# Optimization experiments

Hardware: AMD Instinct MI355X
Metric: run time of the kernel (lower is better)

## Reference

```python
import jax, jax.numpy as jnp
import numpy as np

N, E, D, H = 50000, 800000, 64, 64  # nodes, edges, feat dim, hidden dim
EPS = 1e-3  # Keras BatchNormalization default epsilon

def bn(x, g, b, mu, v):
    # inference-mode batch norm with moving statistics
    return (x - mu) * jax.lax.rsqrt(v + EPS) * g + b

def gelu(x):
    return jax.nn.gelu(x, approximate=False)  # tf.nn.gelu default is exact

def setup_inputs() -> dict:
    key = jax.random.key(0)
    ks = jax.random.split(key, 24)
    r = lambda i, shape, s=1.0: (jax.random.normal(ks[i], shape, jnp.float32) * s)
    inp = {
        "node_feats": r(0, (N, D)),
        "edge_feats": r(1, (E, D)),
        "src": jax.random.randint(ks[2], (E,), 0, N, jnp.int32),
        "dst": jax.random.randint(ks[3], (E,), 0, N, jnp.int32),
        # message MLP (BN -> Dense(gelu)) x2, input D
        "m_g1": 1.0 + 0.1 * r(4, (D,)), "m_b1": 0.1 * r(5, (D,)),
        "m_mu1": 0.1 * r(6, (D,)), "m_v1": jnp.ones((D,), jnp.float32),
        "m_W1": r(7, (D, H), 1.0 / np.sqrt(D)), "m_c1": jnp.zeros((H,), jnp.float32),
        "m_g2": 1.0 + 0.1 * r(8, (H,)), "m_b2": 0.1 * r(9, (H,)),
        "m_mu2": 0.1 * r(10, (H,)), "m_v2": jnp.ones((H,), jnp.float32),
        "m_W2": r(11, (H, H), 1.0 / np.sqrt(H)), "m_c2": jnp.zeros((H,), jnp.float32),
        # edge transformer MLP (Dense(gelu)) x2, input D
        "e_W1": r(12, (D, H), 1.0 / np.sqrt(D)), "e_c1": jnp.zeros((H,), jnp.float32),
        "e_W2": r(13, (H, H), 1.0 / np.sqrt(H)), "e_c2": jnp.zeros((H,), jnp.float32),
        # update MLP (BN -> Dense(gelu)) x2, input D+H (concat combination)
        "u_g1": 1.0 + 0.1 * r(14, (D + H,)), "u_b1": 0.1 * r(15, (D + H,)),
        "u_mu1": 0.1 * r(16, (D + H,)), "u_v1": jnp.ones((D + H,), jnp.float32),
        "u_W1": r(17, (D + H, H), 1.0 / np.sqrt(D + H)), "u_c1": jnp.zeros((H,), jnp.float32),
        "u_g2": 1.0 + 0.1 * r(18, (H,)), "u_b2": 0.1 * r(19, (H,)),
        "u_mu2": 0.1 * r(20, (H,)), "u_v2": jnp.ones((H,), jnp.float32),
        "u_W2": r(21, (H, H), 1.0 / np.sqrt(H)), "u_c2": jnp.zeros((H,), jnp.float32),
    }
    return inp

def reference(node_feats, edge_feats,
              m_g1, m_b1, m_mu1, m_v1, m_W1, m_c1,
              m_g2, m_b2, m_mu2, m_v2, m_W2, m_c2,
              e_W1, e_c1, e_W2, e_c2,
              u_g1, u_b1, u_mu1, u_v1, u_W1, u_c1,
              u_g2, u_b2, u_mu2, u_v2, u_W2, u_c2,
              src, dst):
    # gather neighbour representations: [E, D]
    nbr = node_feats[dst]
    # base message MLP: (BN -> Dropout(identity at inference) -> Dense gelu) x2
    h = gelu(bn(nbr, m_g1, m_b1, m_mu1, m_v1) @ m_W1 + m_c1)
    msg = gelu(bn(h, m_g2, m_b2, m_mu2, m_v2) @ m_W2 + m_c2)
    # edge transformer: Dense(gelu) x2, gates the messages elementwise
    er = gelu(edge_feats @ e_W1 + e_c1)
    er = gelu(er @ e_W2 + e_c2)
    msg = msg * er  # [E, H]
    # unsorted_segment_mean over source node indices (empty segments -> 0)
    s = jax.ops.segment_sum(msg, src, num_segments=N)
    cnt = jax.ops.segment_sum(jnp.ones((E, 1), msg.dtype), src, num_segments=N)
    agg = s / jnp.maximum(cnt, 1.0)  # [N, H]
    # combine ('concat') and update MLP
    hcat = jnp.concatenate([node_feats, agg], axis=-1)  # [N, D+H]
    h = gelu(bn(hcat, u_g1, u_b1, u_mu1, u_v1) @ u_W1 + u_c1)
    out = gelu(bn(h, u_g2, u_b2, u_mu2, u_v2) @ u_W2 + u_c2)
    return out  # [N, H]
```

## Files before the change

kernel.cpp:

```cpp
#include <hip/hip_runtime.h>
#include <hip/hip_bf16.h>

#define NN 50000
#define NE 800000

typedef __bf16 bf16_t;
typedef bf16_t bf16x8 __attribute__((ext_vector_type(8)));
typedef float f32x4 __attribute__((ext_vector_type(4)));

__device__ __forceinline__ float gelu_f(float x) {
    float v = x * fmaf(x * x, 0.07135481627f, 1.595769122f);
    float e = __expf(-v);
    return x * __builtin_amdgcn_rcpf(1.0f + e);
}

__device__ void fold_frag(int K, const float* W, const float* g, const float* b,
                          const float* mu, const float* v, const float* c,
                          bf16_t* Wf, float* cb, int tid, float* part) {
    const int n = tid & 63, kc = tid >> 6;
    const int nt = n >> 4, lrow = n & 15, nkc = K >> 5;
    const int kq = K >> 2, k0 = kc * kq, k1 = k0 + kq;
    float acc = 0.f;
    for (int k = k0; k < k1; ++k) {
        float w = W[k * 64 + n];
        float s = 1.0f, o = 0.0f;
        if (g) {
            s = g[k] * __frsqrt_rn(v[k] + 1e-3f);
            o = b[k] - mu[k] * s;
        }
        int idx = ((nt * nkc + (k >> 5)) * 64 + ((k >> 3) & 3) * 16 + lrow) * 8 + (k & 7);
        Wf[idx] = (bf16_t)(w * s);
        acc += o * w;
    }
    part[kc * 64 + n] = acc;
    __syncthreads();
    if (kc == 0) cb[n] = c[n] + part[n] + part[64 + n] + part[128 + n] + part[192 + n];
}

__global__ void fold_kernel(
    const float* mg1, const float* mb1, const float* mmu1, const float* mv1,
    const float* mW1, const float* mc1,
    const float* mg2, const float* mb2, const float* mmu2, const float* mv2,
    const float* mW2, const float* mc2,
    const float* eW1, const float* ec1, const float* eW2, const float* ec2,
    const float* ug1, const float* ub1, const float* umu1, const float* uv1,
    const float* uW1, const float* uc1,
    const float* ug2, const float* ub2, const float* umu2, const float* uv2,
    const float* uW2, const float* uc2,
    bf16_t* wcat, bf16_t* uW1f, bf16_t* uW2f,
    float* cm1, float* cm2, float* ce1, float* ce2, float* cu1, float* cu2)
{
    __shared__ float part[256];
    int t = threadIdx.x;
    switch (blockIdx.x) {
        case 0: fold_frag(64,  mW1, mg1, mb1, mmu1, mv1, mc1, wcat,         cm1, t, part); break;
        case 1: fold_frag(64,  mW2, mg2, mb2, mmu2, mv2, mc2, wcat + 4096,  cm2, t, part); break;
        case 2: fold_frag(64,  eW1, nullptr, nullptr, nullptr, nullptr, ec1, wcat + 8192,  ce1, t, part); break;
        case 3: fold_frag(64,  eW2, nullptr, nullptr, nullptr, nullptr, ec2, wcat + 12288, ce2, t, part); break;
        case 4: fold_frag(128, uW1, ug1, ub1, umu1, uv1, uc1, uW1f, cu1, t, part); break;
        case 5: fold_frag(64,  uW2, ug2, ub2, umu2, uv2, uc2, uW2f, cu2, t, part); break;
    }
}

__global__ void hist_kernel(const int* __restrict__ src, int* __restrict__ cnt) {
    int e = blockIdx.x * 256 + threadIdx.x;
    if (e < NE) atomicAdd(&cnt[src[e]], 1);
}

__global__ void scanA_kernel(const int* __restrict__ cnt, int* __restrict__ part,
                             int* __restrict__ btot) {
    __shared__ int s[256];
    int tid = threadIdx.x;
    int i = blockIdx.x * 256 + tid;
    int v = (i < NN) ? cnt[i] : 0;
    s[tid] = v;
    __syncthreads();
    #pragma unroll
    for (int off = 1; off < 256; off <<= 1) {
        int t = (tid >= off) ? s[tid - off] : 0;
        __syncthreads();
        s[tid] += t;
        __syncthreads();
    }
    if (i < NN) part[i] = s[tid] - v;
    if (tid == 255) btot[blockIdx.x] = s[255];
}

__global__ void scanB_kernel(int* __restrict__ btot, int nblk) {
    __shared__ int s[256];
    int tid = threadIdx.x;
    int v = (tid < nblk) ? btot[tid] : 0;
    s[tid] = v;
    __syncthreads();
    #pragma unroll
    for (int off = 1; off < 256; off <<= 1) {
        int t = (tid >= off) ? s[tid - off] : 0;
        __syncthreads();
        s[tid] += t;
        __syncthreads();
    }
    if (tid < nblk) btot[tid] = s[tid] - v;
}

__global__ void scanC_kernel(const int* __restrict__ part, const int* __restrict__ btot,
                             int* __restrict__ woff) {
    int i = blockIdx.x * 256 + threadIdx.x;
    if (i < NN) woff[i] = part[i] + btot[i >> 8];
}

__global__ void fill_kernel(const int* __restrict__ src, int* __restrict__ woff,
                            int* __restrict__ elist) {
    int e = blockIdx.x * 256 + threadIdx.x;
    if (e < NE) {
        int pos = atomicAdd(&woff[src[e]], 1);
        elist[pos] = e;
    }
}

__device__ __forceinline__ void mk_frag_hilo(const float* row, int quad,
        bf16x8& hi0, bf16x8& lo0, bf16x8& hi1, bf16x8& lo1)
{
    #pragma unroll
    for (int j = 0; j < 8; ++j) {
        float x0 = row[quad * 8 + j];
        float x1 = row[32 + quad * 8 + j];
        bf16_t h0 = (bf16_t)x0, h1 = (bf16_t)x1;
        hi0[j] = h0; lo0[j] = (bf16_t)(x0 - (float)h0);
        hi1[j] = h1; lo1[j] = (bf16_t)(x1 - (float)h1);
    }
}

__device__ __forceinline__ bf16x8 ldb(const bf16_t* wf, int slot, int lane) {
    return *(const bf16x8*)(wf + (slot * 64 + lane) * 8);
}

__device__ __forceinline__ void gemm64_hilo(const bf16_t* wf, int m,
        bf16x8 h0, bf16x8 l0, bf16x8 h1, bf16x8 l1, f32x4 (&acc)[4], int lane)
{
    #pragma unroll
    for (int nt = 0; nt < 4; ++nt) {
        bf16x8 b0 = ldb(wf, m * 8 + nt * 2 + 0, lane);
        bf16x8 b1 = ldb(wf, m * 8 + nt * 2 + 1, lane);
        f32x4 c = {0.f, 0.f, 0.f, 0.f};
        c = __builtin_amdgcn_mfma_f32_16x16x32_bf16(h0, b0, c, 0, 0, 0);
        c = __builtin_amdgcn_mfma_f32_16x16x32_bf16(l0, b0, c, 0, 0, 0);
        c = __builtin_amdgcn_mfma_f32_16x16x32_bf16(h1, b1, c, 0, 0, 0);
        c = __builtin_amdgcn_mfma_f32_16x16x32_bf16(l1, b1, c, 0, 0, 0);
        acc[nt] = c;
    }
}

__device__ __forceinline__ void gemm64(const bf16_t* wf, int m,
        bf16x8 a0, bf16x8 a1, f32x4 (&acc)[4], int lane)
{
    #pragma unroll
    for (int nt = 0; nt < 4; ++nt) {
        bf16x8 b0 = ldb(wf, m * 8 + nt * 2 + 0, lane);
        bf16x8 b1 = ldb(wf, m * 8 + nt * 2 + 1, lane);
        f32x4 c = {0.f, 0.f, 0.f, 0.f};
        c = __builtin_amdgcn_mfma_f32_16x16x32_bf16(a0, b0, c, 0, 0, 0);
        c = __builtin_amdgcn_mfma_f32_16x16x32_bf16(a1, b1, c, 0, 0, 0);
        acc[nt] = c;
    }
}

__device__ __forceinline__ void epi_to_frag(const f32x4 (&acc)[4], const float* bias,
        bf16_t* h, int lrow, int quad)
{
    #pragma unroll
    for (int nt = 0; nt < 4; ++nt) {
        float bb = bias[nt * 16 + lrow];
        #pragma unroll
        for (int r = 0; r < 4; ++r)
            h[((nt * 2 + (lrow >> 3)) * 16 + quad * 4 + r) * 8 + (lrow & 7)] =
                (bf16_t)gelu_f(acc[nt][r] + bb);
    }
}

__global__ __launch_bounds__(256) void edge_kernel(
    const float* __restrict__ node_feats, const float* __restrict__ edge_feats,
    const int* __restrict__ src, const int* __restrict__ dst,
    const bf16_t* __restrict__ wcat,
    const float* __restrict__ cm1, const float* __restrict__ cm2,
    const float* __restrict__ ce1, const float* __restrict__ ce2,
    float* __restrict__ s_acc, bf16_t* __restrict__ buf, int use_csr)
{
    __shared__ bf16_t wf[16384];
    __shared__ bf16_t hf[4][1024];

    const int tid  = threadIdx.x;
    const int wave = tid >> 6;
    const int lane = tid & 63;
    const int quad = lane >> 4;
    const int lrow = lane & 15;

    #pragma unroll
    for (int i = 0; i < 8; ++i) {
        int chunk = tid + i * 256;
        *(bf16x8*)(wf + chunk * 8) = *(const bf16x8*)(wcat + chunk * 8);
    }
    __syncthreads();

    const int ebase = blockIdx.x * 64 + wave * 16;
    bf16_t* h = hf[wave];

    f32x4 acc[4];

    {
        const float* erow = edge_feats + (size_t)(ebase + lrow) * 64;
        bf16x8 h0, l0, h1, l1;
        mk_frag_hilo(erow, quad, h0, l0, h1, l1);
        gemm64_hilo(wf, 2, h0, l0, h1, l1, acc, lane);
        epi_to_frag(acc, ce1, h, lrow, quad);
    }
    float er[4][4];
    {
        bf16x8 a0 = *(const bf16x8*)(h + lane * 8);
        bf16x8 a1 = *(const bf16x8*)(h + (lane + 64) * 8);
        gemm64(wf, 3, a0, a1, acc, lane);
        #pragma unroll
        for (int nt = 0; nt < 4; ++nt) {
            float bb = ce2[nt * 16 + lrow];
            #pragma unroll
            for (int r = 0; r < 4; ++r) er[nt][r] = gelu_f(acc[nt][r] + bb);
        }
    }

    {
        const int dnode = dst[ebase + lrow];
        const float* nrow = node_feats + (size_t)dnode * 64;
        bf16x8 h0, l0, h1, l1;
        mk_frag_hilo(nrow, quad, h0, l0, h1, l1);
        gemm64_hilo(wf, 0, h0, l0, h1, l1, acc, lane);
        epi_to_frag(acc, cm1, h, lrow, quad);
    }
    float msg[4][4];
    {
        bf16x8 a0 = *(const bf16x8*)(h + lane * 8);
        bf16x8 a1 = *(const bf16x8*)(h + (lane + 64) * 8);
        gemm64(wf, 1, a0, a1, acc, lane);
        #pragma unroll
        for (int nt = 0; nt < 4; ++nt) {
            float bb = cm2[nt * 16 + lrow];
            #pragma unroll
            for (int r = 0; r < 4; ++r) msg[nt][r] = gelu_f(acc[nt][r] + bb);
        }
    }

    if (use_csr) {
        #pragma unroll
        for (int r = 0; r < 4; ++r) {
            bf16_t* bp = buf + (size_t)(ebase + quad * 4 + r) * 64;
            #pragma unroll
            for (int nt = 0; nt < 4; ++nt)
                bp[nt * 16 + lrow] = (bf16_t)(msg[nt][r] * er[nt][r]);
        }
    } else {
        #pragma unroll
        for (int r = 0; r < 4; ++r) {
            float* srow = s_acc + (size_t)src[ebase + quad * 4 + r] * 64;
            #pragma unroll
            for (int nt = 0; nt < 4; ++nt)
                unsafeAtomicAdd(srow + nt * 16 + lrow, msg[nt][r] * er[nt][r]);
        }
    }
}

__global__ __launch_bounds__(256) void agg_kernel(
    const bf16_t* __restrict__ buf, const int* __restrict__ elist,
    const int* __restrict__ woff, const int* __restrict__ cnt,
    float* __restrict__ agg)
{
    const int wave = threadIdx.x >> 6;
    const int lane = threadIdx.x & 63;
    const int n = blockIdx.x * 4 + wave;
    const int deg = cnt[n];
    const int end = woff[n];
    const int start = end - deg;

    float s0 = 0.f, s1 = 0.f, s2 = 0.f, s3 = 0.f;
    int j = start;
    for (; j + 4 <= end; j += 4) {
        int e0 = elist[j], e1 = elist[j + 1], e2 = elist[j + 2], e3 = elist[j + 3];
        s0 += (float)buf[(size_t)e0 * 64 + lane];
        s1 += (float)buf[(size_t)e1 * 64 + lane];
        s2 += (float)buf[(size_t)e2 * 64 + lane];
        s3 += (float)buf[(size_t)e3 * 64 + lane];
    }
    for (; j < end; ++j)
        s0 += (float)buf[(size_t)elist[j] * 64 + lane];

    float r = (deg > 0) ? (s0 + s1 + s2 + s3) * __builtin_amdgcn_rcpf((float)deg) : 0.f;
    agg[(size_t)n * 64 + lane] = r;
}

__global__ __launch_bounds__(256) void update_kernel(
    const float* __restrict__ node_feats,
    const float* __restrict__ aggv, const int* __restrict__ cnt,
    const bf16_t* __restrict__ uW1f, const float* __restrict__ cu1,
    const bf16_t* __restrict__ uW2f, const float* __restrict__ cu2,
    float* __restrict__ out)
{
    __shared__ bf16_t w1f[8192];
    __shared__ bf16_t w2f[4096];
    __shared__ bf16_t hf[4][1024];

    const int tid  = threadIdx.x;
    const int wave = tid >> 6;
    const int lane = tid & 63;
    const int quad = lane >> 4;
    const int lrow = lane & 15;

    #pragma unroll
    for (int i = 0; i < 4; ++i) {
        int chunk = tid + i * 256;
        *(bf16x8*)(w1f + chunk * 8) = *(const bf16x8*)(uW1f + chunk * 8);
    }
    #pragma unroll
    for (int i = 0; i < 2; ++i) {
        int chunk = tid + i * 256;
        *(bf16x8*)(w2f + chunk * 8) = *(const bf16x8*)(uW2f + chunk * 8);
    }
    __syncthreads();

    const int nbase = blockIdx.x * 64 + wave * 16;
    int arow = nbase + lrow;
    arow = arow < NN ? arow : NN - 1;

    const float* nf   = node_feats + (size_t)arow * 64;
    const float* srow = aggv + (size_t)arow * 64;
    float inv = cnt ? 1.0f / fmaxf((float)cnt[arow], 1.0f) : 1.0f;

    bf16x8 ah[4], al[4];
    #pragma unroll
    for (int j = 0; j < 8; ++j) {
        float x0 = nf[quad * 8 + j];
        float x1 = nf[32 + quad * 8 + j];
        float x2 = srow[quad * 8 + j] * inv;
        float x3 = srow[32 + quad * 8 + j] * inv;
        bf16_t h0 = (bf16_t)x0, h1 = (bf16_t)x1, h2 = (bf16_t)x2, h3 = (bf16_t)x3;
        ah[0][j] = h0; al[0][j] = (bf16_t)(x0 - (float)h0);
        ah[1][j] = h1; al[1][j] = (bf16_t)(x1 - (float)h1);
        ah[2][j] = h2; al[2][j] = (bf16_t)(x2 - (float)h2);
        ah[3][j] = h3; al[3][j] = (bf16_t)(x3 - (float)h3);
    }

    f32x4 acc[4];
    #pragma unroll
    for (int nt = 0; nt < 4; ++nt) {
        f32x4 c = {0.f, 0.f, 0.f, 0.f};
        #pragma unroll
        for (int kk = 0; kk < 4; ++kk) {
            bf16x8 b = *(const bf16x8*)(w1f + ((nt * 4 + kk) * 64 + lane) * 8);
            c = __builtin_amdgcn_mfma_f32_16x16x32_bf16(ah[kk], b, c, 0, 0, 0);
            c = __builtin_amdgcn_mfma_f32_16x16x32_bf16(al[kk], b, c, 0, 0, 0);
        }
        acc[nt] = c;
    }
    bf16_t* hb = hf[wave];
    epi_to_frag(acc, cu1, hb, lrow, quad);

    bf16x8 ha0 = *(const bf16x8*)(hb + lane * 8);
    bf16x8 ha1 = *(const bf16x8*)(hb + (lane + 64) * 8);
    gemm64(w2f, 0, ha0, ha1, acc, lane);

    #pragma unroll
    for (int nt = 0; nt < 4; ++nt) {
        int col = nt * 16 + lrow;
        float bb = cu2[col];
        #pragma unroll
        for (int r = 0; r < 4; ++r) {
            int row = nbase + quad * 4 + r;
            if (row < NN)
                out[(size_t)row * 64 + col] = gelu_f(acc[nt][r] + bb);
        }
    }
}

extern "C" void kernel_launch(void* const* d_in, const int* in_sizes, int n_in,
                              void* d_out, int out_size, void* d_ws, size_t ws_size,
                              hipStream_t stream) {
    const float* node_feats = (const float*)d_in[0];
    const float* edge_feats = (const float*)d_in[1];
    const int*   src        = (const int*)d_in[2];
    const int*   dst        = (const int*)d_in[3];

    char* ws = (char*)d_ws;
    const bool csr = ws_size >= (size_t)119200000;

    size_t off = 0;
    bf16_t* buf = nullptr; float* agg = nullptr; int* elist = nullptr;
    int* cnt = nullptr; int* woff = nullptr; int* part = nullptr; int* btot = nullptr;
    float* s_acc = nullptr;

    if (csr) {
        buf   = (bf16_t*)(ws + off); off += (size_t)NE * 64 * 2;
        agg   = (float*)(ws + off);  off += (size_t)NN * 64 * 4;
        elist = (int*)(ws + off);    off += (size_t)NE * 4;
        cnt   = (int*)(ws + off);    off += (size_t)NN * 4;
        woff  = (int*)(ws + off);    off += (size_t)NN * 4;
        part  = (int*)(ws + off);    off += (size_t)NN * 4;
        btot  = (int*)(ws + off);    off += 1024;
    } else {
        s_acc = (float*)(ws + off);  off += (size_t)NN * 64 * 4;
        cnt   = (int*)(ws + off);    off += (size_t)NN * 4;
    }
    bf16_t* wcat = (bf16_t*)(ws + off); off += 32768;
    bf16_t* uW1f = (bf16_t*)(ws + off); off += 16384;
    bf16_t* uW2f = (bf16_t*)(ws + off); off += 8192;
    float* cm1 = (float*)(ws + off); off += 256;
    float* cm2 = (float*)(ws + off); off += 256;
    float* ce1 = (float*)(ws + off); off += 256;
    float* ce2 = (float*)(ws + off); off += 256;
    float* cu1 = (float*)(ws + off); off += 256;
    float* cu2 = (float*)(ws + off); off += 256;

    if (csr) {
        hipMemsetAsync(cnt, 0, (size_t)NN * 4, stream);
    } else {
        hipMemsetAsync(s_acc, 0, (size_t)NN * 64 * 4 + (size_t)NN * 4, stream);
    }

    fold_kernel<<<6, 256, 0, stream>>>(
        (const float*)d_in[4],  (const float*)d_in[5],  (const float*)d_in[6],  (const float*)d_in[7],
        (const float*)d_in[8],  (const float*)d_in[9],
        (const float*)d_in[10], (const float*)d_in[11], (const float*)d_in[12], (const float*)d_in[13],
        (const float*)d_in[14], (const float*)d_in[15],
        (const float*)d_in[16], (const float*)d_in[17], (const float*)d_in[18], (const float*)d_in[19],
        (const float*)d_in[20], (const float*)d_in[21], (const float*)d_in[22], (const float*)d_in[23],
        (const float*)d_in[24], (const float*)d_in[25],
        (const float*)d_in[26], (const float*)d_in[27], (const float*)d_in[28], (const float*)d_in[29],
        (const float*)d_in[30], (const float*)d_in[31],
        wcat, uW1f, uW2f, cm1, cm2, ce1, ce2, cu1, cu2);

    hist_kernel<<<(NE + 255) / 256, 256, 0, stream>>>(src, cnt);

    if (csr) {
        const int NBLK = (NN + 255) / 256;
        scanA_kernel<<<NBLK, 256, 0, stream>>>(cnt, part, btot);
        scanB_kernel<<<1, 256, 0, stream>>>(btot, NBLK);
        scanC_kernel<<<NBLK, 256, 0, stream>>>(part, btot, woff);
        fill_kernel<<<(NE + 255) / 256, 256, 0, stream>>>(src, woff, elist);
    }

    edge_kernel<<<NE / 64, 256, 0, stream>>>(
        node_feats, edge_feats, src, dst,
        wcat, cm1, cm2, ce1, ce2, s_acc, buf, csr ? 1 : 0);

    if (csr) {
        agg_kernel<<<NN / 4, 256, 0, stream>>>(buf, elist, woff, cnt, agg);
        update_kernel<<<(NN + 63) / 64, 256, 0, stream>>>(
            node_feats, agg, nullptr, uW1f, cu1, uW2f, cu2, (float*)d_out);
    } else {
        update_kernel<<<(NN + 63) / 64, 256, 0, stream>>>(
            node_feats, s_acc, cnt, uW1f, cu1, uW2f, cu2, (float*)d_out);
    }
}
```

Baseline: 563.5 us.

## Compute message MLP per node and scatter edge outputs into CSR order

The message MLP depends only on the destination node's features, so a new node_msg_kernel computes it once per node (50k rows instead of 800k edges) and stores it as bf16. The edge kernel then gathers that precomputed bf16 message, runs only the edge-transformer MLP, and writes the gated product straight to its CSR slot using a per-edge position from fill_kernel. The aggregation kernel can then read contiguous rows with no edge-list indirection. In exchange the node messages are rounded to bf16 before gating, and pos and msg share workspace with agg.

```diff
diff --git a/kernel.cpp b/kernel.cpp
--- a/kernel.cpp
+++ b/kernel.cpp
@@ -109,12 +109,9 @@
 }
 
 __global__ void fill_kernel(const int* __restrict__ src, int* __restrict__ woff,
-                            int* __restrict__ elist) {
+                            int* __restrict__ pos) {
     int e = blockIdx.x * 256 + threadIdx.x;
-    if (e < NE) {
-        int pos = atomicAdd(&woff[src[e]], 1);
-        elist[pos] = e;
-    }
+    if (e < NE) pos[e] = atomicAdd(&woff[src[e]], 1);
 }
 
 __device__ __forceinline__ void mk_frag_hilo(const float* row, int quad,
@@ -177,15 +174,12 @@
     }
 }
 
-__global__ __launch_bounds__(256) void edge_kernel(
-    const float* __restrict__ node_feats, const float* __restrict__ edge_feats,
-    const int* __restrict__ src, const int* __restrict__ dst,
-    const bf16_t* __restrict__ wcat,
+__global__ __launch_bounds__(256) void node_msg_kernel(
+    const float* __restrict__ node_feats, const bf16_t* __restrict__ wcat,
     const float* __restrict__ cm1, const float* __restrict__ cm2,
-    const float* __restrict__ ce1, const float* __restrict__ ce2,
-    float* __restrict__ s_acc, bf16_t* __restrict__ buf, int use_csr)
-{
-    __shared__ bf16_t wf[16384];
+    bf16_t* __restrict__ msg)
+{
+    __shared__ bf16_t wf[8192];
     __shared__ bf16_t hf[4][1024];
 
     const int tid  = threadIdx.x;
@@ -195,81 +189,121 @@
     const int lrow = lane & 15;
 
     #pragma unroll
-    for (int i = 0; i < 8; ++i) {
+    for (int i = 0; i < 4; ++i) {
         int chunk = tid + i * 256;
         *(bf16x8*)(wf + chunk * 8) = *(const bf16x8*)(wcat + chunk * 8);
     }
     __syncthreads();
 
+    const int nbase = blockIdx.x * 64 + wave * 16;
+    int arow = nbase + lrow;
+    arow = arow < NN ? arow : NN - 1;
+
+    f32x4 acc[4];
+    {
+        const float* nrow = node_feats + (size_t)arow * 64;
+        bf16x8 h0, l0, h1, l1;
+        mk_frag_hilo(nrow, quad, h0, l0, h1, l1);
+        gemm64_hilo(wf, 0, h0, l0, h1, l1, acc, lane);
+        epi_to_frag(acc, cm1, hf[wave], lrow, quad);
+    }
+    bf16x8 a0 = *(const bf16x8*)(hf[wave] + lane * 8);
+    bf16x8 a1 = *(const bf16x8*)(hf[wave] + (lane + 64) * 8);
+    gemm64(wf, 1, a0, a1, acc, lane);
+
+    #pragma unroll
+    for (int nt = 0; nt < 4; ++nt) {
+        float bb = cm2[nt * 16 + lrow];
+        #pragma unroll
+        for (int r = 0; r < 4; ++r) {
+            int row = nbase + quad * 4 + r;
+            if (row < NN)
+                msg[(size_t)row * 64 + nt * 16 + lrow] = (bf16_t)gelu_f(acc[nt][r] + bb);
+        }
+    }
+}
+
+__global__ __launch_bounds__(256) void edge_kernel(
+    const float* __restrict__ edge_feats,
+    const int* __restrict__ src, const int* __restrict__ dst,
+    const int* __restrict__ pos,
+    const bf16_t* __restrict__ wcat,
+    const float* __restrict__ ce1, const float* __restrict__ ce2,
+    const bf16_t* __restrict__ msg,
+    float* __restrict__ s_acc, bf16_t* __restrict__ buf, int use_csr)
+{
+    __shared__ bf16_t wf[8192];
+    __shared__ bf16_t hf[4][1024];
+
+    const int tid  = threadIdx.x;
+    const int wave = tid >> 6;
+    const int lane = tid & 63;
+    const int quad = lane >> 4;
+    const int lrow = lane & 15;
+
+    #pragma unroll
+    for (int i = 0; i < 4; ++i) {
+        int chunk = tid + i * 256;
+        *(bf16x8*)(wf + chunk * 8) = *(const bf16x8*)(wcat + 8192 + chunk * 8);
+    }
+    __syncthreads();
+
     const int ebase = blockIdx.x * 64 + wave * 16;
     bf16_t* h = hf[wave];
 
+    int erow_id[4];
+    #pragma unroll
+    for (int r = 0; r < 4; ++r) erow_id[r] = ebase + quad * 4 + r;
+    bf16_t mg[4][4];
+    #pragma unroll
+    for (int r = 0; r < 4; ++r) {
+        const bf16_t* mrow = msg + (size_t)dst[erow_id[r]] * 64;
+        #pragma unroll
+        for (int nt = 0; nt < 4; ++nt) mg[r][nt] = mrow[nt * 16 + lrow];
+    }
+
     f32x4 acc[4];
-
     {
-        const float* erow = edge_feats + (size_t)(ebase + lrow) * 64;
+        const float* efr = edge_feats + (size_t)(ebase + lrow) * 64;
         bf16x8 h0, l0, h1, l1;
-        mk_frag_hilo(erow, quad, h0, l0, h1, l1);
-        gemm64_hilo(wf, 2, h0, l0, h1, l1, acc, lane);
+        mk_frag_hilo(efr, quad, h0, l0, h1, l1);
+        gemm64_hilo(wf, 0, h0, l0, h1, l1, acc, lane);
         epi_to_frag(acc, ce1, h, lrow, quad);
     }
-    float er[4][4];
-    {
-        bf16x8 a0 = *(const bf16x8*)(h + lane * 8);
-        bf16x8 a1 = *(const bf16x8*)(h + (lane + 64) * 8);
-        gemm64(wf, 3, a0, a1, acc, lane);
+    bf16x8 a0 = *(const bf16x8*)(h + lane * 8);
+    bf16x8 a1 = *(const bf16x8*)(h + (lane + 64) * 8);
+    gemm64(wf, 1, a0, a1, acc, lane);
+
+    if (use_csr) {
+        int pe[4];
+        #pragma unroll
+        for (int r = 0; r < 4; ++r) pe[r] = pos[erow_id[r]];
         #pragma unroll
         for (int nt = 0; nt < 4; ++nt) {
             float bb = ce2[nt * 16 + lrow];
             #pragma unroll
-            for (int r = 0; r < 4; ++r) er[nt][r] = gelu_f(acc[nt][r] + bb);
-        }
-    }
-
-    {
-        const int dnode = dst[ebase + lrow];
-        const float* nrow = node_feats + (size_t)dnode * 64;
-        bf16x8 h0, l0, h1, l1;
-        mk_frag_hilo(nrow, quad, h0, l0, h1, l1);
-        gemm64_hilo(wf, 0, h0, l0, h1, l1, acc, lane);
-        epi_to_frag(acc, cm1, h, lrow, quad);
-    }
-    float msg[4][4];
-    {
-        bf16x8 a0 = *(const bf16x8*)(h + lane * 8);
-        bf16x8 a1 = *(const bf16x8*)(h + (lane + 64) * 8);
-        gemm64(wf, 1, a0, a1, acc, lane);
+            for (int r = 0; r < 4; ++r) {
+                float er = gelu_f(acc[nt][r] + bb);
+                buf[(size_t)pe[r] * 64 + nt * 16 + lrow] = (bf16_t)(er * (float)mg[r][nt]);
+            }
+        }
+    } else {
         #pragma unroll
         for (int nt = 0; nt < 4; ++nt) {
-            float bb = cm2[nt * 16 + lrow];
+            float bb = ce2[nt * 16 + lrow];
             #pragma unroll
-            for (int r = 0; r < 4; ++r) msg[nt][r] = gelu_f(acc[nt][r] + bb);
-        }
-    }
-
-    if (use_csr) {
-        #pragma unroll
-        for (int r = 0; r < 4; ++r) {
-            bf16_t* bp = buf + (size_t)(ebase + quad * 4 + r) * 64;
-            #pragma unroll
-            for (int nt = 0; nt < 4; ++nt)
-                bp[nt * 16 + lrow] = (bf16_t)(msg[nt][r] * er[nt][r]);
-        }
-    } else {
-        #pragma unroll
-        for (int r = 0; r < 4; ++r) {
-            float* srow = s_acc + (size_t)src[ebase + quad * 4 + r] * 64;
-            #pragma unroll
-            for (int nt = 0; nt < 4; ++nt)
-                unsafeAtomicAdd(srow + nt * 16 + lrow, msg[nt][r] * er[nt][r]);
+            for (int r = 0; r < 4; ++r) {
+                float er = gelu_f(acc[nt][r] + bb);
+                unsafeAtomicAdd(&s_acc[(size_t)src[erow_id[r]] * 64 + nt * 16 + lrow],
+                                er * (float)mg[r][nt]);
+            }
         }
     }
 }
 
 __global__ __launch_bounds__(256) void agg_kernel(
-    const bf16_t* __restrict__ buf, const int* __restrict__ elist,
-    const int* __restrict__ woff, const int* __restrict__ cnt,
-    float* __restrict__ agg)
+    const bf16_t* __restrict__ buf, const int* __restrict__ woff,
+    const int* __restrict__ cnt, float* __restrict__ agg)
 {
     const int wave = threadIdx.x >> 6;
     const int lane = threadIdx.x & 63;
@@ -279,16 +313,16 @@
     const int start = end - deg;
 
     float s0 = 0.f, s1 = 0.f, s2 = 0.f, s3 = 0.f;
+    const bf16_t* p = buf + (size_t)start * 64 + lane;
     int j = start;
     for (; j + 4 <= end; j += 4) {
-        int e0 = elist[j], e1 = elist[j + 1], e2 = elist[j + 2], e3 = elist[j + 3];
-        s0 += (float)buf[(size_t)e0 * 64 + lane];
-        s1 += (float)buf[(size_t)e1 * 64 + lane];
-        s2 += (float)buf[(size_t)e2 * 64 + lane];
-        s3 += (float)buf[(size_t)e3 * 64 + lane];
-    }
-    for (; j < end; ++j)
-        s0 += (float)buf[(size_t)elist[j] * 64 + lane];
+        s0 += (float)p[0];
+        s1 += (float)p[64];
+        s2 += (float)p[128];
+        s3 += (float)p[192];
+        p += 256;
+    }
+    for (; j < end; ++j) { s0 += (float)p[0]; p += 64; }
 
     float r = (deg > 0) ? (s0 + s1 + s2 + s3) * __builtin_amdgcn_rcpf((float)deg) : 0.f;
     agg[(size_t)n * 64 + lane] = r;
@@ -386,24 +420,27 @@
     const int*   dst        = (const int*)d_in[3];
 
     char* ws = (char*)d_ws;
-    const bool csr = ws_size >= (size_t)119200000;
+    const bool csr = ws_size >= (size_t)116500000;
 
     size_t off = 0;
-    bf16_t* buf = nullptr; float* agg = nullptr; int* elist = nullptr;
-    int* cnt = nullptr; int* woff = nullptr; int* part = nullptr; int* btot = nullptr;
-    float* s_acc = nullptr;
+    bf16_t* buf = nullptr; float* agg = nullptr; int* pos = nullptr; bf16_t* msg = nullptr;
+    float* s_acc = nullptr; int* cnt = nullptr; int* woff = nullptr;
+    int* part = nullptr; int* btot = nullptr;
 
     if (csr) {
-        buf   = (bf16_t*)(ws + off); off += (size_t)NE * 64 * 2;
-        agg   = (float*)(ws + off);  off += (size_t)NN * 64 * 4;
-        elist = (int*)(ws + off);    off += (size_t)NE * 4;
+        buf = (bf16_t*)(ws + off); off += (size_t)NE * 128;
+        char* aggbase = ws + off;
+        agg = (float*)aggbase;     off += (size_t)NN * 256;
+        pos = (int*)aggbase;
+        msg = (bf16_t*)(aggbase + (size_t)NE * 4);
+        cnt  = (int*)(ws + off); off += (size_t)NN * 4;
+        woff = (int*)(ws + off); off += (size_t)NN * 4;
+        part = (int*)(ws + off); off += (size_t)NN * 4;
+        btot = (int*)(ws + off); off += 1024;
+    } else {
+        s_acc = (float*)(ws + off);  off += (size_t)NN * 256;
         cnt   = (int*)(ws + off);    off += (size_t)NN * 4;
-        woff  = (int*)(ws + off);    off += (size_t)NN * 4;
-        part  = (int*)(ws + off);    off += (size_t)NN * 4;
-        btot  = (int*)(ws + off);    off += 1024;
-    } else {
-        s_acc = (float*)(ws + off);  off += (size_t)NN * 64 * 4;
-        cnt   = (int*)(ws + off);    off += (size_t)NN * 4;
+        msg   = (bf16_t*)(ws + off); off += (size_t)NN * 128;
     }
     bf16_t* wcat = (bf16_t*)(ws + off); off += 32768;
     bf16_t* uW1f = (bf16_t*)(ws + off); off += 16384;
@@ -418,7 +455,7 @@
     if (csr) {
         hipMemsetAsync(cnt, 0, (size_t)NN * 4, stream);
     } else {
-        hipMemsetAsync(s_acc, 0, (size_t)NN * 64 * 4 + (size_t)NN * 4, stream);
+        hipMemsetAsync(s_acc, 0, (size_t)NN * 256 + (size_t)NN * 4, stream);
     }
 
     fold_kernel<<<6, 256, 0, stream>>>(
@@ -433,6 +470,8 @@
         (const float*)d_in[30], (const float*)d_in[31],
         wcat, uW1f, uW2f, cm1, cm2, ce1, ce2, cu1, cu2);
 
+    node_msg_kernel<<<(NN + 63) / 64, 256, 0, stream>>>(node_feats, wcat, cm1, cm2, msg);
+
     hist_kernel<<<(NE + 255) / 256, 256, 0, stream>>>(src, cnt);
 
     if (csr) {
@@ -440,15 +479,14 @@
         scanA_kernel<<<NBLK, 256, 0, stream>>>(cnt, part, btot);
         scanB_kernel<<<1, 256, 0, stream>>>(btot, NBLK);
         scanC_kernel<<<NBLK, 256, 0, stream>>>(part, btot, woff);
-        fill_kernel<<<(NE + 255) / 256, 256, 0, stream>>>(src, woff, elist);
+        fill_kernel<<<(NE + 255) / 256, 256, 0, stream>>>(src, woff, pos);
     }
 
     edge_kernel<<<NE / 64, 256, 0, stream>>>(
-        node_feats, edge_feats, src, dst,
-        wcat, cm1, cm2, ce1, ce2, s_acc, buf, csr ? 1 : 0);
+        edge_feats, src, dst, pos, wcat, ce1, ce2, msg, s_acc, buf, csr ? 1 : 0);
 
     if (csr) {
-        agg_kernel<<<NN / 4, 256, 0, stream>>>(buf, elist, woff, cnt, agg);
+        agg_kernel<<<NN / 4, 256, 0, stream>>>(buf, woff, cnt, agg);
         update_kernel<<<(NN + 63) / 64, 256, 0, stream>>>(
             node_feats, agg, nullptr, uW1f, cu1, uW2f, cu2, (float*)d_out);
     } else {
```

Result: faster. 519.5 us (-7.8%).
